# Kernel tuning notes

Hardware: AMD Instinct MI355X
Metric: run time of the kernel (lower is better)

Reference implementation:

```python
import jax, jax.numpy as jnp
import numpy as np

DIM = 1024
HEADS = 16
SCALE = DIM ** -0.5  # note: source scales by full dim, not head dim


def setup_inputs() -> dict:
    key = jax.random.key(0)
    k1, k2, k3 = jax.random.split(key, 3)
    b, n = 2, 2048
    x = jax.random.normal(k1, (b, n, DIM), dtype=jnp.float32)
    w_qkv = jax.random.normal(k2, (3 * DIM, DIM), dtype=jnp.float32) * (DIM ** -0.5)
    w_out = jax.random.normal(k3, (DIM, DIM), dtype=jnp.float32) * (DIM ** -0.5)
    b_out = jnp.zeros((DIM,), dtype=jnp.float32)
    return {"x": x, "w_qkv": w_qkv, "w_out": w_out, "b_out": b_out}


def reference(x, w_qkv, w_out, b_out):
    b, n, d = x.shape
    h = HEADS
    hd = d // h
    # torch Linear: y = x @ W.T
    qkv = x @ w_qkv.T  # [b, n, 3d]
    q, k, v = jnp.split(qkv, 3, axis=-1)
    # reshape to [b, h, n, hd]
    def to_heads(t):
        return t.reshape(b, n, h, hd).transpose(0, 2, 1, 3)
    q, k, v = to_heads(q), to_heads(k), to_heads(v)
    dots = jnp.einsum('bhqd,bhkd->bhqk', q, k) * SCALE
    attn = jax.nn.softmax(dots, axis=-1)
    out = jnp.einsum('bhqk,bhkd->bhqd', attn, v)
    out = out.transpose(0, 2, 1, 3).reshape(b, n, d)
    return out @ w_out.T + b_out
```

## Files before the change

kernel.cpp:

```cpp
#include <hip/hip_runtime.h>

typedef __attribute__((ext_vector_type(8))) _Float16 half8;
typedef __attribute__((ext_vector_type(4))) _Float16 half4;
typedef __attribute__((ext_vector_type(2))) __fp16 fp16x2;
typedef __attribute__((ext_vector_type(4))) float f32x4;
typedef __attribute__((ext_vector_type(4))) unsigned int u32x4;
typedef __attribute__((ext_vector_type(2))) unsigned int u32x2;

#define NSEQ 2048
#define DIMM 1024
#define NH   16
#define HD   64

typedef const void __attribute__((address_space(1))) gvoid_t;
typedef void __attribute__((address_space(3))) svoid_t;

__device__ __forceinline__ void gload_lds16(const void* g, void* l) {
  __builtin_amdgcn_global_load_lds((gvoid_t*)g, (svoid_t*)l, 16, 0, 0);
}

union H2U { fp16x2 h; unsigned int u; };

__global__ __launch_bounds__(256) void cvt_all(const float* __restrict__ x,
                                               const float* __restrict__ wqkv,
                                               const float* __restrict__ wout,
                                               _Float16* __restrict__ xh,
                                               _Float16* __restrict__ wqkvh,
                                               _Float16* __restrict__ wouth) {
  int i = blockIdx.x * 256 + threadIdx.x;
  const float* src;
  _Float16* dst;
  int off;
  if (i < 524288) { src = x; dst = xh; off = i; }
  else if (i < 917504) { src = wqkv; dst = wqkvh; off = i - 524288; }
  else { src = wout; dst = wouth; off = i - 917504; }
  const float4* p = (const float4*)src + (size_t)off * 2;
  float4 v0 = p[0], v1 = p[1];
  half8 h;
  h[0] = (_Float16)v0.x; h[1] = (_Float16)v0.y; h[2] = (_Float16)v0.z; h[3] = (_Float16)v0.w;
  h[4] = (_Float16)v1.x; h[5] = (_Float16)v1.y; h[6] = (_Float16)v1.z; h[7] = (_Float16)v1.w;
  *((half8*)dst + off) = h;
}

__device__ __forceinline__ void gemm_mainloop(const _Float16* __restrict__ A,
                                              const _Float16* __restrict__ B,
                                              int am0, int bn0,
                                              _Float16* As, _Float16* Bs,
                                              f32x4 acc[4][4]) {
  const int tid = threadIdx.x;
  const int w = tid >> 6, lane = tid & 63;
  const int lr = lane >> 2;
  const int lc = (lane & 3) * 8;
  const int wm = (w >> 1) * 64, wn = (w & 1) * 64;
  const int g = lane >> 4, ln = lane & 15;

  for (int k0 = 0; k0 < 1024; k0 += 32) {
#pragma unroll
    for (int rr = 0; rr < 4; ++rr) {
      int c = rr * 4 + w;
      if (c < 8) {
        gload_lds16(A + (size_t)(am0 + c * 16 + lr) * 1024 + k0 + lc, As + c * 512);
      } else {
        int cb = c - 8;
        gload_lds16(B + (size_t)(bn0 + cb * 16 + lr) * 1024 + k0 + lc, Bs + cb * 512);
      }
    }
    __syncthreads();
    half8 af[4], bf[4];
#pragma unroll
    for (int mi = 0; mi < 4; ++mi)
      af[mi] = *(const half8*)(As + (wm + mi * 16 + ln) * 32 + g * 8);
#pragma unroll
    for (int ni = 0; ni < 4; ++ni)
      bf[ni] = *(const half8*)(Bs + (wn + ni * 16 + ln) * 32 + g * 8);
#pragma unroll
    for (int mi = 0; mi < 4; ++mi)
#pragma unroll
      for (int ni = 0; ni < 4; ++ni)
        acc[mi][ni] = __builtin_amdgcn_mfma_f32_16x16x32_f16(af[mi], bf[ni], acc[mi][ni], 0, 0, 0);
    __syncthreads();
  }
}

union SmemQKV {
  struct { _Float16 a[128 * 32]; _Float16 b[128 * 32]; } ab;
  _Float16 t[128 * 136];
};

#define QSCALE 0.0450843450f

__global__ __launch_bounds__(256) void gemm_qkv(const _Float16* __restrict__ x,
                                                const _Float16* __restrict__ wqkv,
                                                _Float16* __restrict__ qh,
                                                _Float16* __restrict__ kh,
                                                _Float16* __restrict__ vt) {
  __shared__ SmemQKV sh;
  f32x4 acc[4][4];
#pragma unroll
  for (int i = 0; i < 4; ++i)
#pragma unroll
    for (int j = 0; j < 4; ++j) acc[i][j] = (f32x4){0.f, 0.f, 0.f, 0.f};
  const int bm = blockIdx.x, bn = blockIdx.y;
  gemm_mainloop(x, wqkv, bm * 128, bn * 128, sh.ab.a, sh.ab.b, acc);

  const int tid = threadIdx.x;
  const int w = tid >> 6, lane = tid & 63;
  const int g = lane >> 4, ln = lane & 15;
  const int wm = (w >> 1) * 64, wn = (w & 1) * 64;
  const int sec = bn >> 3;
  const int cbase = (bn & 7) * 128;

  if (sec < 2) {
    _Float16* dst = (sec == 0) ? qh : kh;
    const float scale = (sec == 0) ? QSCALE : 1.0f;
#pragma unroll
    for (int mi = 0; mi < 4; ++mi) {
      int row = bm * 128 + wm + mi * 16 + g * 4;
      int bidx = row >> 11, nidx = row & 2047;
#pragma unroll
      for (int ni = 0; ni < 4; ++ni) {
        int col = cbase + wn + ni * 16 + ln;
        int h = col >> 6, d = col & 63;
        _Float16* p = dst + ((size_t)(bidx * NH + h) * NSEQ + nidx) * HD + d;
#pragma unroll
        for (int r = 0; r < 4; ++r) p[r * HD] = (_Float16)(acc[mi][ni][r] * scale);
      }
    }
  } else {
    __syncthreads();
#pragma unroll
    for (int mi = 0; mi < 4; ++mi)
#pragma unroll
      for (int ni = 0; ni < 4; ++ni)
#pragma unroll
        for (int r = 0; r < 4; ++r)
          sh.t[(wn + ni * 16 + ln) * 136 + wm + mi * 16 + g * 4 + r] = (_Float16)acc[mi][ni][r];
    __syncthreads();
    const int row0 = bm * 128;
    const int bidx = row0 >> 11, n0 = row0 & 2047;
#pragma unroll
    for (int i = 0; i < 8; ++i) {
      int ci = i * 256 + tid;
      int drow = ci >> 4, nofs = (ci & 15) * 8;
      int col = cbase + drow;
      int h = col >> 6, d = col & 63;
      u32x4 val = *(const u32x4*)(sh.t + drow * 136 + nofs);
      *(u32x4*)(vt + ((size_t)(bidx * NH + h) * HD + d) * NSEQ + n0 + nofs) = val;
    }
  }
}

__global__ __launch_bounds__(256, 2) void attn_fwd(const _Float16* __restrict__ qg,
                                                   const _Float16* __restrict__ kg,
                                                   const _Float16* __restrict__ vg,
                                                   _Float16* __restrict__ ao) {
  __shared__ _Float16 Ks[3][64 * 64];
  __shared__ _Float16 Vs[3][64 * 64];

  const int bid = blockIdx.x;
  const int swz = (bid & 7) * 64 + (bid >> 3);
  const int bh = swz >> 4, qt = swz & 15;
  const int tid = threadIdx.x, w = tid >> 6, lane = tid & 63;
  const int g = lane >> 4, ln = lane & 15;
  const int sw8 = ln & 7;

  const _Float16* qp = qg + (size_t)bh * NSEQ * HD;
  const _Float16* kp = kg + (size_t)bh * NSEQ * HD;
  const _Float16* vp = vg + (size_t)bh * HD * NSEQ;

  const int qr = qt * 128 + w * 32;

  half8 qf[2][2];
#pragma unroll
  for (int qb = 0; qb < 2; ++qb)
#pragma unroll
    for (int dk = 0; dk < 2; ++dk)
      qf[qb][dk] = *(const half8*)(qp + (size_t)(qr + qb * 16 + ln) * HD + dk * 32 + g * 8);
  asm volatile("" ::: "memory");

  const int rsub = lane >> 3;
  const int csw = ((lane & 7) ^ rsub) << 3;
  const int c0 = 2 * w;
  const int R0 = c0 * 8 + rsub, R1 = R0 + 8;
  const int ks0 = 32 * (R0 >> 5) + 8 * ((R0 >> 2) & 3) + 4 * ((R0 >> 4) & 1) + (R0 & 3);
  const int ks1 = 32 * (R1 >> 5) + 8 * ((R1 >> 2) & 3) + 4 * ((R1 >> 4) & 1) + (R1 & 3);

#define STAGE(buf, tt)                                                              \
  {                                                                                 \
    const _Float16* kt_ = kp + (size_t)(tt) * 64 * HD;                              \
    gload_lds16(kt_ + (size_t)ks0 * HD + csw, &Ks[buf][c0 * 512]);                  \
    gload_lds16(kt_ + (size_t)ks1 * HD + csw, &Ks[buf][(c0 + 1) * 512]);            \
    gload_lds16(vp + (size_t)(c0 * 8 + rsub) * NSEQ + (tt) * 64 + csw,              \
                &Vs[buf][c0 * 512]);                                                \
    gload_lds16(vp + (size_t)((c0 + 1) * 8 + rsub) * NSEQ + (tt) * 64 + csw,        \
                &Vs[buf][(c0 + 1) * 512]);                                          \
  }

  STAGE(0, 0);
  STAGE(1, 1);

  float lsum[2] = {0.f, 0.f};
  f32x4 oacc[4][2];
#pragma unroll
  for (int sd = 0; sd < 4; ++sd)
#pragma unroll
    for (int qb = 0; qb < 2; ++qb) oacc[sd][qb] = (f32x4){0.f, 0.f, 0.f, 0.f};
  const f32x4 fz = (f32x4){0.f, 0.f, 0.f, 0.f};

#define TILE_BODY(kbuf, vbuf)                                                       \
  {                                                                                 \
    const _Float16* kb_ = (kbuf);                                                   \
    const _Float16* vb_ = (vbuf);                                                   \
    f32x4 sacc[4][2];                                                               \
    __builtin_amdgcn_s_setprio(1);                                                  \
    _Pragma("unroll")                                                               \
    for (int s = 0; s < 4; ++s) {                                                   \
      const _Float16* kr = kb_ + (s * 16 + ln) * 64;                                \
      half8 kf0 = *(const half8*)(kr + ((g ^ sw8) << 3));                           \
      half8 kf1 = *(const half8*)(kr + (((4 + g) ^ sw8) << 3));                     \
      sacc[s][0] = __builtin_amdgcn_mfma_f32_16x16x32_f16(kf0, qf[0][0], fz, 0, 0, 0);            \
      sacc[s][0] = __builtin_amdgcn_mfma_f32_16x16x32_f16(kf1, qf[0][1], sacc[s][0], 0, 0, 0);    \
      sacc[s][1] = __builtin_amdgcn_mfma_f32_16x16x32_f16(kf0, qf[1][0], fz, 0, 0, 0);            \
      sacc[s][1] = __builtin_amdgcn_mfma_f32_16x16x32_f16(kf1, qf[1][1], sacc[s][1], 0, 0, 0);    \
    }                                                                               \
    __builtin_amdgcn_s_setprio(0);                                                  \
    half8 vf[4][2];                                                                 \
    _Pragma("unroll")                                                               \
    for (int sd = 0; sd < 4; ++sd) {                                                \
      const _Float16* vr = vb_ + (sd * 16 + ln) * 64;                               \
      vf[sd][0] = *(const half8*)(vr + ((g ^ sw8) << 3));                           \
      vf[sd][1] = *(const half8*)(vr + (((4 + g) ^ sw8) << 3));                     \
    }                                                                               \
    half8 pb[2][2];                                                                 \
    _Pragma("unroll")                                                               \
    for (int qb = 0; qb < 2; ++qb) {                                                \
      float e[4][4];                                                                \
      float rs = 0.f;                                                               \
      _Pragma("unroll")                                                             \
      for (int s = 0; s < 4; ++s) {                                                 \
        e[s][0] = __builtin_amdgcn_exp2f(sacc[s][qb][0]);                           \
        e[s][1] = __builtin_amdgcn_exp2f(sacc[s][qb][1]);                           \
        e[s][2] = __builtin_amdgcn_exp2f(sacc[s][qb][2]);                           \
        e[s][3] = __builtin_amdgcn_exp2f(sacc[s][qb][3]);                           \
        rs += (e[s][0] + e[s][1]) + (e[s][2] + e[s][3]);                            \
      }                                                                             \
      lsum[qb] += rs;                                                               \
      H2U c00, c01, c10, c11, c20, c21, c30, c31;                                   \
      c00.h = __builtin_amdgcn_cvt_pkrtz(e[0][0], e[0][1]);                         \
      c01.h = __builtin_amdgcn_cvt_pkrtz(e[0][2], e[0][3]);                         \
      c10.h = __builtin_amdgcn_cvt_pkrtz(e[1][0], e[1][1]);                         \
      c11.h = __builtin_amdgcn_cvt_pkrtz(e[1][2], e[1][3]);                         \
      c20.h = __builtin_amdgcn_cvt_pkrtz(e[2][0], e[2][1]);                         \
      c21.h = __builtin_amdgcn_cvt_pkrtz(e[2][2], e[2][3]);                         \
      c30.h = __builtin_amdgcn_cvt_pkrtz(e[3][0], e[3][1]);                         \
      c31.h = __builtin_amdgcn_cvt_pkrtz(e[3][2], e[3][3]);                         \
      union { u32x4 u; half8 h; } p0, p1;                                           \
      p0.u[0] = c00.u; p0.u[1] = c01.u; p0.u[2] = c10.u; p0.u[3] = c11.u;           \
      p1.u[0] = c20.u; p1.u[1] = c21.u; p1.u[2] = c30.u; p1.u[3] = c31.u;           \
      pb[qb][0] = p0.h;                                                             \
      pb[qb][1] = p1.h;                                                             \
    }                                                                               \
    __builtin_amdgcn_s_setprio(1);                                                  \
    _Pragma("unroll")                                                               \
    for (int sd = 0; sd < 4; ++sd) {                                                \
      _Pragma("unroll")                                                             \
      for (int qb = 0; qb < 2; ++qb) {                                              \
        oacc[sd][qb] = __builtin_amdgcn_mfma_f32_16x16x32_f16(vf[sd][0], pb[qb][0], oacc[sd][qb], 0, 0, 0); \
        oacc[sd][qb] = __builtin_amdgcn_mfma_f32_16x16x32_f16(vf[sd][1], pb[qb][1], oacc[sd][qb], 0, 0, 0); \
      }                                                                             \
    }                                                                               \
    __builtin_amdgcn_s_setprio(0);                                                  \
  }

  for (int t = 0; t < 30; ++t) {
    asm volatile("s_waitcnt vmcnt(4)" ::: "memory");
    __builtin_amdgcn_s_barrier();
    STAGE((t + 2) % 3, t + 2);
    TILE_BODY(&Ks[t % 3][0], &Vs[t % 3][0])
  }
  {
    asm volatile("s_waitcnt vmcnt(4)" ::: "memory");
    __builtin_amdgcn_s_barrier();
    TILE_BODY(&Ks[0][0], &Vs[0][0])
  }
  {
    asm volatile("s_waitcnt vmcnt(0)" ::: "memory");
    __builtin_amdgcn_s_barrier();
    TILE_BODY(&Ks[1][0], &Vs[1][0])
  }

  const int bidx = bh >> 4, h = bh & 15;
#pragma unroll
  for (int qb = 0; qb < 2; ++qb) {
    lsum[qb] += __shfl_xor(lsum[qb], 16, 64);
    lsum[qb] += __shfl_xor(lsum[qb], 32, 64);
    const float inv = 1.f / lsum[qb];
    const int n = qr + qb * 16 + ln;
#pragma unroll
    for (int sd = 0; sd < 4; ++sd) {
      half4 o4;
#pragma unroll
      for (int r = 0; r < 4; ++r) o4[r] = (_Float16)(oacc[sd][qb][r] * inv);
      *(half4*)(ao + (size_t)(bidx * NSEQ + n) * DIMM + h * HD + sd * 16 + g * 4) = o4;
    }
  }
}

__global__ __launch_bounds__(256) void gemm_out(const _Float16* __restrict__ ao,
                                                const _Float16* __restrict__ wout,
                                                const float* __restrict__ bias,
                                                float* __restrict__ out) {
  __shared__ _Float16 As[128 * 32];
  __shared__ _Float16 Bs[128 * 32];
  f32x4 acc[4][4];
#pragma unroll
  for (int i = 0; i < 4; ++i)
#pragma unroll
    for (int j = 0; j < 4; ++j) acc[i][j] = (f32x4){0.f, 0.f, 0.f, 0.f};
  const int bm = blockIdx.x, bn = blockIdx.y;
  gemm_mainloop(ao, wout, bm * 128, bn * 128, As, Bs, acc);
  const int tid = threadIdx.x;
  const int w = tid >> 6, lane = tid & 63;
  const int g = lane >> 4, ln = lane & 15;
  const int wm = (w >> 1) * 64, wn = (w & 1) * 64;
#pragma unroll
  for (int mi = 0; mi < 4; ++mi) {
    const int row = bm * 128 + wm + mi * 16 + g * 4;
#pragma unroll
    for (int ni = 0; ni < 4; ++ni) {
      const int col = bn * 128 + wn + ni * 16 + ln;
      const float b = bias[col];
#pragma unroll
      for (int r = 0; r < 4; ++r) out[(size_t)(row + r) * DIMM + col] = acc[mi][ni][r] + b;
    }
  }
}

extern "C" void kernel_launch(void* const* d_in, const int* in_sizes, int n_in,
                              void* d_out, int out_size, void* d_ws, size_t ws_size,
                              hipStream_t stream) {
  const float* x    = (const float*)d_in[0];
  const float* wqkv = (const float*)d_in[1];
  const float* wout = (const float*)d_in[2];
  const float* bout = (const float*)d_in[3];
  float* out = (float*)d_out;

  _Float16* ws = (_Float16*)d_ws;
  _Float16* x_h    = ws;
  _Float16* wqkv_h = ws + (4u << 20);
  _Float16* wout_h = ws + (7u << 20);
  _Float16* q_h    = ws + (8u << 20);
  _Float16* k_h    = ws + (12u << 20);
  _Float16* vt_h   = ws + (16u << 20);
  _Float16* ao_h   = ws + (20u << 20);

  cvt_all<<<dim3(4096), 256, 0, stream>>>(x, wqkv, wout, x_h, wqkv_h, wout_h);
  gemm_qkv<<<dim3(32, 24), 256, 0, stream>>>(x_h, wqkv_h, q_h, k_h, vt_h);
  attn_fwd<<<dim3(512), 256, 0, stream>>>(q_h, k_h, vt_h, ao_h);
  gemm_out<<<dim3(32, 8), 256, 0, stream>>>(ao_h, wout_h, bout, out);
}
```

Measured before the change: 107.7 us.

## Split attention warps 2x2 over query and key halves with LDS output reduction

Each warp in the attention kernel now handles 64 query rows against half of each 64-key tile, instead of 32 query rows against the full tile. The goal is to halve the per-warp LDS reads of K and V fragments per MFMA by reusing each loaded key and value fragment across more query blocks. The two key-half partial outputs and row sums are merged at the end through shared memory, reusing the K buffer as float scratch. This doubles the accumulator and Q-fragment register footprint. The scratch area is larger than the K buffer, so it relies on V being laid out right after K.

```diff
diff --git a/kernel.cpp b/kernel.cpp
--- a/kernel.cpp
+++ b/kernel.cpp
@@ -156,6 +156,7 @@
                                                    _Float16* __restrict__ ao) {
   __shared__ _Float16 Ks[3][64 * 64];
   __shared__ _Float16 Vs[3][64 * 64];
+  __shared__ float Lred[2][128];
 
   const int bid = blockIdx.x;
   const int swz = (bid & 7) * 64 + (bid >> 3);
@@ -163,19 +164,20 @@
   const int tid = threadIdx.x, w = tid >> 6, lane = tid & 63;
   const int g = lane >> 4, ln = lane & 15;
   const int sw8 = ln & 7;
+  const int qh2 = w >> 1, kh2 = w & 1;
 
   const _Float16* qp = qg + (size_t)bh * NSEQ * HD;
   const _Float16* kp = kg + (size_t)bh * NSEQ * HD;
   const _Float16* vp = vg + (size_t)bh * HD * NSEQ;
 
-  const int qr = qt * 128 + w * 32;
-
-  half8 qf[2][2];
-#pragma unroll
-  for (int qb = 0; qb < 2; ++qb)
+  const int qr0 = qt * 128;
+
+  half8 qf[4][2];
+#pragma unroll
+  for (int qb = 0; qb < 4; ++qb)
 #pragma unroll
     for (int dk = 0; dk < 2; ++dk)
-      qf[qb][dk] = *(const half8*)(qp + (size_t)(qr + qb * 16 + ln) * HD + dk * 32 + g * 8);
+      qf[qb][dk] = *(const half8*)(qp + (size_t)(qr0 + qh2 * 64 + qb * 16 + ln) * HD + dk * 32 + g * 8);
   asm volatile("" ::: "memory");
 
   const int rsub = lane >> 3;
@@ -199,76 +201,64 @@
   STAGE(0, 0);
   STAGE(1, 1);
 
-  float lsum[2] = {0.f, 0.f};
-  f32x4 oacc[4][2];
+  float lsum[4] = {0.f, 0.f, 0.f, 0.f};
+  f32x4 oacc[4][4];
 #pragma unroll
   for (int sd = 0; sd < 4; ++sd)
 #pragma unroll
-    for (int qb = 0; qb < 2; ++qb) oacc[sd][qb] = (f32x4){0.f, 0.f, 0.f, 0.f};
+    for (int qb = 0; qb < 4; ++qb) oacc[sd][qb] = (f32x4){0.f, 0.f, 0.f, 0.f};
   const f32x4 fz = (f32x4){0.f, 0.f, 0.f, 0.f};
 
 #define TILE_BODY(kbuf, vbuf)                                                       \
   {                                                                                 \
     const _Float16* kb_ = (kbuf);                                                   \
     const _Float16* vb_ = (vbuf);                                                   \
-    f32x4 sacc[4][2];                                                               \
+    f32x4 sacc[2][4];                                                  \
     __builtin_amdgcn_s_setprio(1);                                                  \
     _Pragma("unroll")                                                               \
-    for (int s = 0; s < 4; ++s) {                                                   \
-      const _Float16* kr = kb_ + (s * 16 + ln) * 64;                                \
+    for (int s = 0; s < 2; ++s) {                                                   \
+      const _Float16* kr = kb_ + (kh2 * 32 + s * 16 + ln) * 64;                     \
       half8 kf0 = *(const half8*)(kr + ((g ^ sw8) << 3));                           \
       half8 kf1 = *(const half8*)(kr + (((4 + g) ^ sw8) << 3));                     \
-      sacc[s][0] = __builtin_amdgcn_mfma_f32_16x16x32_f16(kf0, qf[0][0], fz, 0, 0, 0);            \
-      sacc[s][0] = __builtin_amdgcn_mfma_f32_16x16x32_f16(kf1, qf[0][1], sacc[s][0], 0, 0, 0);    \
-      sacc[s][1] = __builtin_amdgcn_mfma_f32_16x16x32_f16(kf0, qf[1][0], fz, 0, 0, 0);            \
-      sacc[s][1] = __builtin_amdgcn_mfma_f32_16x16x32_f16(kf1, qf[1][1], sacc[s][1], 0, 0, 0);    \
+      _Pragma("unroll")                                                             \
+      for (int qb = 0; qb < 4; ++qb) {                                              \
+        sacc[s][qb] = __builtin_amdgcn_mfma_f32_16x16x32_f16(kf0, qf[qb][0], fz, 0, 0, 0);          \
+        sacc[s][qb] = __builtin_amdgcn_mfma_f32_16x16x32_f16(kf1, qf[qb][1], sacc[s][qb], 0, 0, 0); \
+      }                                                                             \
     }                                                                               \
     __builtin_amdgcn_s_setprio(0);                                                  \
-    half8 vf[4][2];                                                                 \
+    half8 vf[4];                          \
     _Pragma("unroll")                                                               \
-    for (int sd = 0; sd < 4; ++sd) {                                                \
-      const _Float16* vr = vb_ + (sd * 16 + ln) * 64;                               \
-      vf[sd][0] = *(const half8*)(vr + ((g ^ sw8) << 3));                           \
-      vf[sd][1] = *(const half8*)(vr + (((4 + g) ^ sw8) << 3));                     \
-    }                                                                               \
-    half8 pb[2][2];                                                                 \
+    for (int sd = 0; sd < 4; ++sd)                                                  \
+      vf[sd] = *(const half8*)(vb_ + (sd * 16 + ln) * 64 +                          \
+                               (((kh2 * 4 + g) ^ sw8) << 3));                       \
+    half8 pb[4];                                                                    \
     _Pragma("unroll")                                                               \
-    for (int qb = 0; qb < 2; ++qb) {                                                \
-      float e[4][4];                                                                \
-      float rs = 0.f;                                                               \
-      _Pragma("unroll")                                                             \
-      for (int s = 0; s < 4; ++s) {                                                 \
-        e[s][0] = __builtin_amdgcn_exp2f(sacc[s][qb][0]);                           \
-        e[s][1] = __builtin_amdgcn_exp2f(sacc[s][qb][1]);                           \
-        e[s][2] = __builtin_amdgcn_exp2f(sacc[s][qb][2]);                           \
-        e[s][3] = __builtin_amdgcn_exp2f(sacc[s][qb][3]);                           \
-        rs += (e[s][0] + e[s][1]) + (e[s][2] + e[s][3]);                            \
-      }                                                                             \
-      lsum[qb] += rs;                                                               \
-      H2U c00, c01, c10, c11, c20, c21, c30, c31;                                   \
-      c00.h = __builtin_amdgcn_cvt_pkrtz(e[0][0], e[0][1]);                         \
-      c01.h = __builtin_amdgcn_cvt_pkrtz(e[0][2], e[0][3]);                         \
-      c10.h = __builtin_amdgcn_cvt_pkrtz(e[1][0], e[1][1]);                         \
-      c11.h = __builtin_amdgcn_cvt_pkrtz(e[1][2], e[1][3]);                         \
-      c20.h = __builtin_amdgcn_cvt_pkrtz(e[2][0], e[2][1]);                         \
-      c21.h = __builtin_amdgcn_cvt_pkrtz(e[2][2], e[2][3]);                         \
-      c30.h = __builtin_amdgcn_cvt_pkrtz(e[3][0], e[3][1]);                         \
-      c31.h = __builtin_amdgcn_cvt_pkrtz(e[3][2], e[3][3]);                         \
-      union { u32x4 u; half8 h; } p0, p1;                                           \
-      p0.u[0] = c00.u; p0.u[1] = c01.u; p0.u[2] = c10.u; p0.u[3] = c11.u;           \
-      p1.u[0] = c20.u; p1.u[1] = c21.u; p1.u[2] = c30.u; p1.u[3] = c31.u;           \
-      pb[qb][0] = p0.h;                                                             \
-      pb[qb][1] = p1.h;                                                             \
+    for (int qb = 0; qb < 4; ++qb) {                                                \
+      float e0 = __builtin_amdgcn_exp2f(sacc[0][qb][0]);                            \
+      float e1 = __builtin_amdgcn_exp2f(sacc[0][qb][1]);                            \
+      float e2 = __builtin_amdgcn_exp2f(sacc[0][qb][2]);                            \
+      float e3 = __builtin_amdgcn_exp2f(sacc[0][qb][3]);                            \
+      float e4 = __builtin_amdgcn_exp2f(sacc[1][qb][0]);                            \
+      float e5 = __builtin_amdgcn_exp2f(sacc[1][qb][1]);                            \
+      float e6 = __builtin_amdgcn_exp2f(sacc[1][qb][2]);                            \
+      float e7 = __builtin_amdgcn_exp2f(sacc[1][qb][3]);                            \
+      lsum[qb] += ((e0 + e1) + (e2 + e3)) + ((e4 + e5) + (e6 + e7));                \
+      H2U c0_, c1_, c2_, c3_;                                                       \
+      c0_.h = __builtin_amdgcn_cvt_pkrtz(e0, e1);                                   \
+      c1_.h = __builtin_amdgcn_cvt_pkrtz(e2, e3);                                   \
+      c2_.h = __builtin_amdgcn_cvt_pkrtz(e4, e5);                                   \
+      c3_.h = __builtin_amdgcn_cvt_pkrtz(e6, e7);                                   \
+      union { u32x4 u; half8 h; } pk;                                               \
+      pk.u[0] = c0_.u; pk.u[1] = c1_.u; pk.u[2] = c2_.u; pk.u[3] = c3_.u;           \
+      pb[qb] = pk.h;                                                                \
     }                                                                               \
     __builtin_amdgcn_s_setprio(1);                                                  \
     _Pragma("unroll")                                                               \
-    for (int sd = 0; sd < 4; ++sd) {                                                \
+    for (int sd = 0; sd < 4; ++sd)                                                  \
       _Pragma("unroll")                                                             \
-      for (int qb = 0; qb < 2; ++qb) {                                              \
-        oacc[sd][qb] = __builtin_amdgcn_mfma_f32_16x16x32_f16(vf[sd][0], pb[qb][0], oacc[sd][qb], 0, 0, 0); \
-        oacc[sd][qb] = __builtin_amdgcn_mfma_f32_16x16x32_f16(vf[sd][1], pb[qb][1], oacc[sd][qb], 0, 0, 0); \
-      }                                                                             \
-    }                                                                               \
+      for (int qb = 0; qb < 4; ++qb)                                                \
+        oacc[sd][qb] = __builtin_amdgcn_mfma_f32_16x16x32_f16(vf[sd], pb[qb], oacc[sd][qb], 0, 0, 0); \
     __builtin_amdgcn_s_setprio(0);                                                  \
   }
 
@@ -289,19 +279,41 @@
     TILE_BODY(&Ks[1][0], &Vs[1][0])
   }
 
-  const int bidx = bh >> 4, h = bh & 15;
-#pragma unroll
-  for (int qb = 0; qb < 2; ++qb) {
+#pragma unroll
+  for (int qb = 0; qb < 4; ++qb) {
     lsum[qb] += __shfl_xor(lsum[qb], 16, 64);
     lsum[qb] += __shfl_xor(lsum[qb], 32, 64);
-    const float inv = 1.f / lsum[qb];
-    const int n = qr + qb * 16 + ln;
-#pragma unroll
-    for (int sd = 0; sd < 4; ++sd) {
-      half4 o4;
-#pragma unroll
-      for (int r = 0; r < 4; ++r) o4[r] = (_Float16)(oacc[sd][qb][r] * inv);
-      *(half4*)(ao + (size_t)(bidx * NSEQ + n) * DIMM + h * HD + sd * 16 + g * 4) = o4;
+  }
+  __syncthreads();
+  float* Osh = (float*)&Ks[0][0];
+  if (g == 0) {
+#pragma unroll
+    for (int qb = 0; qb < 4; ++qb)
+      Lred[kh2][qh2 * 64 + qb * 16 + ln] = lsum[qb];
+  }
+  if (kh2) {
+#pragma unroll
+    for (int sd = 0; sd < 4; ++sd)
+#pragma unroll
+      for (int qb = 0; qb < 4; ++qb)
+        *(f32x4*)&Osh[(qh2 * 64 + qb * 16 + ln) * 66 + sd * 16 + g * 4] = oacc[sd][qb];
+  }
+  __syncthreads();
+  if (!kh2) {
+    const int bidx = bh >> 4, h = bh & 15;
+#pragma unroll
+    for (int qb = 0; qb < 4; ++qb) {
+      const int q = qh2 * 64 + qb * 16 + ln;
+      const float inv = 1.f / (Lred[0][q] + Lred[1][q]);
+      const int n = qr0 + q;
+#pragma unroll
+      for (int sd = 0; sd < 4; ++sd) {
+        f32x4 part = *(const f32x4*)&Osh[q * 66 + sd * 16 + g * 4];
+        half4 o4;
+#pragma unroll
+        for (int r = 0; r < 4; ++r) o4[r] = (_Float16)((oacc[sd][qb][r] + part[r]) * inv);
+        *(half4*)(ao + (size_t)(bidx * NSEQ + n) * DIMM + h * HD + sd * 16 + g * 4) = o4;
+      }
     }
   }
 }
```

After: 108.2 us. About the same (+0.5%).
